# Optimization experiments

Hardware: AMD Instinct MI355X
Metric: run time of the kernel (lower is better)

## Reference

```python
import jax, jax.numpy as jnp
import numpy as np

N_NODES = 200000
N_EDGES = 3200000
NUM_GRAPHS = 100
WIN = 30
H1, H2, OUT = 500, 20, 4


def setup_inputs() -> dict:
    key = jax.random.key(0)
    ks = jax.random.split(key, 8)
    features = jax.random.normal(ks[0], (N_NODES, WIN), dtype=jnp.float32)
    src = jax.random.randint(ks[1], (N_EDGES,), 0, N_NODES, dtype=jnp.int32)
    dst = jax.random.randint(ks[2], (N_EDGES,), 0, N_NODES, dtype=jnp.int32)
    # contiguous equal-size graphs: 2000 nodes per graph -> ids sorted 0..99
    graph_ids = (jnp.arange(N_NODES, dtype=jnp.int32) // (N_NODES // NUM_GRAPHS))
    W1 = jax.random.normal(ks[3], (WIN, H1), dtype=jnp.float32) / np.sqrt(WIN)
    b1 = jnp.zeros((H1,), jnp.float32)
    W2 = jax.random.normal(ks[4], (H1, H2), dtype=jnp.float32) / np.sqrt(H1)
    b2 = jnp.zeros((H2,), jnp.float32)
    W3 = jax.random.normal(ks[5], (H2, OUT), dtype=jnp.float32) / np.sqrt(H2)
    b3 = jnp.zeros((OUT,), jnp.float32)
    return {"features": features, "src": src, "dst": dst, "graph_ids": graph_ids,
            "num_graphs": NUM_GRAPHS, "W1": W1, "b1": b1, "W2": W2, "b2": b2,
            "W3": W3, "b3": b3}


def reference(features, src, dst, graph_ids, num_graphs, W1, b1, W2, b2, W3, b3):
    N = features.shape[0]
    ones = jnp.ones(src.shape[0], dtype=features.dtype)
    # DGL GraphConv norm='both': D_out^{-1/2} on src side, D_in^{-1/2} on dst side
    deg_out = jnp.maximum(jax.ops.segment_sum(ones, src, num_segments=N), 1.0)
    deg_in = jnp.maximum(jax.ops.segment_sum(ones, dst, num_segments=N), 1.0)
    x = features * jax.lax.rsqrt(deg_out)[:, None]
    # aggregate first (in_feats < out_feats), then dense transform
    agg = jax.ops.segment_sum(x[src], dst, num_segments=N)          # [N, 30]
    agg = agg * jax.lax.rsqrt(deg_in)[:, None]
    h = jax.nn.silu(agg @ W1 + b1)                                   # [N, 500]
    pooled = jax.ops.segment_max(h, graph_ids, num_segments=num_graphs)  # [G, 500]
    y = jax.nn.silu(pooled @ W2 + b2)                                # dropout = identity (eval)
    return jax.nn.sigmoid(y @ W3 + b3)                               # [G, 4]
```

## Files before the change

kernel.cpp:

```cpp
#include <hip/hip_runtime.h>
#include <hip/hip_fp16.h>

#define WIN 30
#define H1 500
#define H1P 512
#define H2 20
#define OUTD 4
#define CS 4
#define NBIN 61440
#define NBINW (NBIN/4)
#define NCH 48
#define RPB 512
#define MAXPB 9216
#define BINCHUNK 8192
#define NBMAX 400

typedef _Float16 f16x8 __attribute__((ext_vector_type(8)));
typedef float f32x4 __attribute__((ext_vector_type(4)));

__global__ __launch_bounds__(1024) void k_hb(const int* __restrict__ src,
                                             const int* __restrict__ dst,
                                             unsigned* __restrict__ partial,
                                             int* __restrict__ gcur,
                                             unsigned* __restrict__ ebuf,
                                             int E, int NB, int NHB) {
    __shared__ unsigned h[NBINW];
    const int tid = threadIdx.x;
    if ((int)blockIdx.x < NHB) {
        const int r = blockIdx.x / NCH, c = blockIdx.x % NCH;
        const int nbase = r * NBIN;
        for (int j = tid; j < NBINW; j += 1024) h[j] = 0;
        __syncthreads();
        const int ce = ((E + NCH - 1) / NCH + 3) & ~3;
        const int start = c * ce;
        const int end = min(E, start + ce);
        for (int i = start + tid * 4; i < end; i += 1024 * 4) {
            if (i + 3 < end) {
                int4 s4 = *(const int4*)(src + i);
                unsigned d;
                d = (unsigned)(s4.x - nbase); if (d < NBIN) atomicAdd(&h[d >> 2], 1u << ((d & 3) * 8));
                d = (unsigned)(s4.y - nbase); if (d < NBIN) atomicAdd(&h[d >> 2], 1u << ((d & 3) * 8));
                d = (unsigned)(s4.z - nbase); if (d < NBIN) atomicAdd(&h[d >> 2], 1u << ((d & 3) * 8));
                d = (unsigned)(s4.w - nbase); if (d < NBIN) atomicAdd(&h[d >> 2], 1u << ((d & 3) * 8));
            } else {
                for (int k = i; k < end; ++k) {
                    unsigned d = (unsigned)(src[k] - nbase);
                    if (d < NBIN) atomicAdd(&h[d >> 2], 1u << ((d & 3) * 8));
                }
            }
        }
        __syncthreads();
        unsigned* outp = partial + (size_t)blockIdx.x * NBINW;
        for (int j = tid; j < NBINW; j += 1024) outp[j] = h[j];
    } else {
        int* cnt = (int*)h;
        int* base = (int*)h + NBMAX;
        const int bb = blockIdx.x - NHB;
        for (int j = tid; j < NB; j += 1024) cnt[j] = 0;
        __syncthreads();
        const int start = bb * BINCHUNK;
        const int end = min(E, start + BINCHUNK);
        for (int i = start + tid; i < end; i += 1024)
            atomicAdd(&cnt[dst[i] >> 9], 1);
        __syncthreads();
        for (int j = tid; j < NB; j += 1024) {
            int c = cnt[j];
            base[j] = j * MAXPB + (c ? atomicAdd(&gcur[j], c) : 0);
            cnt[j] = 0;
        }
        __syncthreads();
        for (int i = start + tid; i < end; i += 1024) {
            int d = dst[i];
            int b = d >> 9;
            int idx = atomicAdd(&cnt[b], 1);
            int pos = base[b] + idx;
            if (pos < (b + 1) * MAXPB)
                ebuf[pos] = ((unsigned)src[i] << 9) | (unsigned)(d & 511);
        }
    }
}

__global__ __launch_bounds__(256) void k_prep2(const unsigned* __restrict__ partial,
                                               const float* __restrict__ feat,
                                               const float* __restrict__ W1,
                                               __half* __restrict__ xh,
                                               __half* __restrict__ w1cm,
                                               int N, int nmb) {
    const int tid = threadIdx.x;
    if ((int)blockIdx.x == nmb) {
        for (int i = tid; i < H1P * 32; i += 256) {
            int c = i >> 5, k = i & 31;
            float v = (k < WIN && c < H1) ? W1[k * H1 + c] : 0.f;
            w1cm[i] = __float2half(v);
        }
        return;
    }
    __shared__ float rs[1024];
    {
        int w = blockIdx.x * 256 + tid;
        int node0 = 4 * w;
        int r = node0 / NBIN;
        int lw = (node0 - r * NBIN) >> 2;
        const unsigned* p = partial + (size_t)(r * NCH) * NBINW + lw;
        unsigned b0 = 0, b1 = 0, b2 = 0, b3 = 0;
        for (int c = 0; c < NCH; ++c) {
            unsigned v = p[(size_t)c * NBINW];
            b0 += v & 0xFFu; b1 += (v >> 8) & 0xFFu;
            b2 += (v >> 16) & 0xFFu; b3 += v >> 24;
        }
        rs[tid * 4 + 0] = rsqrtf((float)max((int)b0, 1));
        rs[tid * 4 + 1] = rsqrtf((float)max((int)b1, 1));
        rs[tid * 4 + 2] = rsqrtf((float)max((int)b2, 1));
        rs[tid * 4 + 3] = rsqrtf((float)max((int)b3, 1));
    }
    __syncthreads();
    const int nbase = blockIdx.x * 1024;
    for (int task = tid; task < 1024 * 4; task += 256) {
        int node_l = task >> 2;
        int node = nbase + node_l;
        if (node >= N) break;
        int c8 = (task & 3) * 8;
        float r = rs[node_l];
        float f[8];
#pragma unroll
        for (int q = 0; q < 8; ++q) {
            int d = c8 + q;
            f[q] = (d < WIN) ? feat[(size_t)node * WIN + d] * r : 0.f;
        }
        union { uint4 u4; __half2 h2[4]; } y;
        y.h2[0] = __floats2half2_rn(f[0], f[1]);
        y.h2[1] = __floats2half2_rn(f[2], f[3]);
        y.h2[2] = __floats2half2_rn(f[4], f[5]);
        y.h2[3] = __floats2half2_rn(f[6], f[7]);
        *(uint4*)(xh + (size_t)node * 32 + c8) = y.u4;
    }
}

__global__ __launch_bounds__(1024) void k_agg(const __half* __restrict__ xh,
                                              const unsigned* __restrict__ ebuf,
                                              const int* __restrict__ gcur,
                                              __half* __restrict__ agg, int N) {
    __shared__ unsigned es[MAXPB];
    __shared__ int cnt[RPB + 1];
    __shared__ int cur[RPB];
    const int tid = threadIdx.x;
    const int b = blockIdx.x;
    for (int j = tid; j < RPB; j += 1024) { cnt[j + 1] = 0; cur[j] = 0; }
    if (tid == 0) cnt[0] = 0;
    __syncthreads();
    const int ne = min(gcur[b], MAXPB);
    const unsigned* eb = ebuf + (size_t)b * MAXPB;
    for (int i = tid; i < ne; i += 1024)
        atomicAdd(&cnt[(int)(eb[i] & (RPB - 1)) + 1], 1);
    __syncthreads();
    if (tid < 64) {
        const int i0 = tid * 8;
        int s[8];
        int run = 0;
#pragma unroll
        for (int k = 0; k < 8; ++k) { run += cnt[i0 + k + 1]; s[k] = run; }
        int inc = run;
#pragma unroll
        for (int o = 1; o < 64; o <<= 1) {
            int u = __shfl_up(inc, o, 64);
            if (tid >= o) inc += u;
        }
        const int ex = inc - run;
#pragma unroll
        for (int k = 0; k < 8; ++k) cnt[i0 + k + 1] = ex + s[k];
    }
    __syncthreads();
    for (int i = tid; i < ne; i += 1024) {
        unsigned p = eb[i];
        int ld = (int)(p & (RPB - 1));
        int idx = atomicAdd(&cur[ld], 1);
        es[cnt[ld] + idx] = p;
    }
    __syncthreads();
    for (int task = tid; task < RPB * 4; task += 1024) {
        const int node_l = task >> 2;
        const int c8 = (task & 3) * 8;
        const int o0 = cnt[node_l], o1 = cnt[node_l + 1];
        float a0 = 0.f, a1 = 0.f, a2 = 0.f, a3 = 0.f;
        float a4 = 0.f, a5 = 0.f, a6 = 0.f, a7 = 0.f;
        int j = o0;
        for (; j + 3 < o1; j += 4) {
            unsigned p0 = es[j], p1 = es[j + 1], p2 = es[j + 2], p3 = es[j + 3];
            union { uint4 u4; __half2 h2[4]; } x0, x1, x2, x3;
            x0.u4 = *(const uint4*)(xh + (size_t)(p0 >> 9) * 32 + c8);
            x1.u4 = *(const uint4*)(xh + (size_t)(p1 >> 9) * 32 + c8);
            x2.u4 = *(const uint4*)(xh + (size_t)(p2 >> 9) * 32 + c8);
            x3.u4 = *(const uint4*)(xh + (size_t)(p3 >> 9) * 32 + c8);
            a0 += __low2float(x0.h2[0]) + __low2float(x1.h2[0]) + __low2float(x2.h2[0]) + __low2float(x3.h2[0]);
            a1 += __high2float(x0.h2[0]) + __high2float(x1.h2[0]) + __high2float(x2.h2[0]) + __high2float(x3.h2[0]);
            a2 += __low2float(x0.h2[1]) + __low2float(x1.h2[1]) + __low2float(x2.h2[1]) + __low2float(x3.h2[1]);
            a3 += __high2float(x0.h2[1]) + __high2float(x1.h2[1]) + __high2float(x2.h2[1]) + __high2float(x3.h2[1]);
            a4 += __low2float(x0.h2[2]) + __low2float(x1.h2[2]) + __low2float(x2.h2[2]) + __low2float(x3.h2[2]);
            a5 += __high2float(x0.h2[2]) + __high2float(x1.h2[2]) + __high2float(x2.h2[2]) + __high2float(x3.h2[2]);
            a6 += __low2float(x0.h2[3]) + __low2float(x1.h2[3]) + __low2float(x2.h2[3]) + __low2float(x3.h2[3]);
            a7 += __high2float(x0.h2[3]) + __high2float(x1.h2[3]) + __high2float(x2.h2[3]) + __high2float(x3.h2[3]);
        }
        for (; j < o1; ++j) {
            unsigned p0 = es[j];
            union { uint4 u4; __half2 h2[4]; } x0;
            x0.u4 = *(const uint4*)(xh + (size_t)(p0 >> 9) * 32 + c8);
            a0 += __low2float(x0.h2[0]);  a1 += __high2float(x0.h2[0]);
            a2 += __low2float(x0.h2[1]);  a3 += __high2float(x0.h2[1]);
            a4 += __low2float(x0.h2[2]);  a5 += __high2float(x0.h2[2]);
            a6 += __low2float(x0.h2[3]);  a7 += __high2float(x0.h2[3]);
        }
        const int node = b * RPB + node_l;
        if (node < N) {
            float deg = (float)(o1 - o0);
            float r = rsqrtf(fmaxf(deg, 1.f));
            union { uint4 u4; __half2 h2[4]; } y;
            y.h2[0] = __floats2half2_rn(a0 * r, a1 * r);
            y.h2[1] = __floats2half2_rn(a2 * r, a3 * r);
            y.h2[2] = __floats2half2_rn(a4 * r, a5 * r);
            y.h2[3] = __floats2half2_rn(a6 * r, a7 * r);
            *(uint4*)(agg + (size_t)node * 32 + c8) = y.u4;
        }
    }
}

__global__ __launch_bounds__(256) void k_gemm(const __half* __restrict__ agg,
                                              const __half* __restrict__ w1cm,
                                              const float* __restrict__ b1,
                                              float* __restrict__ pooled,
                                              int NPG, int G) {
    const int bid = blockIdx.x;
    const int g = bid / CS, c = bid % CS;
    const int tid = threadIdx.x;
    const int w = tid >> 6;
    const int l = tid & 63;
    const int lo = l & 15, hi = l >> 4;

    f16x8 bfr[8];
#pragma unroll
    for (int ct = 0; ct < 8; ++ct) {
        int col = c * 128 + ct * 16 + lo;
        bfr[ct] = *(const f16x8*)(w1cm + (size_t)col * 32 + hi * 8);
    }
    float vmax[8], vmin[8];
#pragma unroll
    for (int ct = 0; ct < 8; ++ct) { vmax[ct] = -INFINITY; vmin[ct] = INFINITY; }

    const int mts = NPG >> 4;
    for (int mt = w; mt < mts; mt += 4) {
        int node = g * NPG + mt * 16 + lo;
        f16x8 a = *(const f16x8*)(agg + (size_t)node * 32 + hi * 8);
#pragma unroll
        for (int ct = 0; ct < 8; ++ct) {
            f32x4 acc = {0.f, 0.f, 0.f, 0.f};
            acc = __builtin_amdgcn_mfma_f32_16x16x32_f16(a, bfr[ct], acc, 0, 0, 0);
#pragma unroll
            for (int q = 0; q < 4; ++q) {
                vmax[ct] = fmaxf(vmax[ct], acc[q]);
                vmin[ct] = fminf(vmin[ct], acc[q]);
            }
        }
    }
#pragma unroll
    for (int ct = 0; ct < 8; ++ct) {
        vmax[ct] = fmaxf(vmax[ct], __shfl_xor(vmax[ct], 16, 64));
        vmax[ct] = fmaxf(vmax[ct], __shfl_xor(vmax[ct], 32, 64));
        vmin[ct] = fminf(vmin[ct], __shfl_xor(vmin[ct], 16, 64));
        vmin[ct] = fminf(vmin[ct], __shfl_xor(vmin[ct], 32, 64));
    }
    __shared__ float red[2][4][8][16];
    if (hi == 0) {
#pragma unroll
        for (int ct = 0; ct < 8; ++ct) {
            red[0][w][ct][lo] = vmax[ct];
            red[1][w][ct][lo] = vmin[ct];
        }
    }
    __syncthreads();
    if (tid < 128) {
        int ct = tid >> 4, col16 = tid & 15;
        float m = fmaxf(fmaxf(red[0][0][ct][col16], red[0][1][ct][col16]),
                        fmaxf(red[0][2][ct][col16], red[0][3][ct][col16]));
        float n = fminf(fminf(red[1][0][ct][col16], red[1][1][ct][col16]),
                        fminf(red[1][2][ct][col16], red[1][3][ct][col16]));
        int col = c * 128 + ct * 16 + col16;
        float bb = (col < H1) ? b1[col] : 0.f;
        m += bb; n += bb;
        float sm = m / (1.f + __expf(-m));
        float sn = n / (1.f + __expf(-n));
        pooled[(size_t)g * H1P + col] = fmaxf(sm, sn);
    }
}

__global__ __launch_bounds__(64) void k_head(const float* __restrict__ pooled,
                                             const float* __restrict__ W2,
                                             const float* __restrict__ b2,
                                             const float* __restrict__ W3,
                                             const float* __restrict__ b3,
                                             float* __restrict__ out, int G) {
    const int g = blockIdx.x;
    const int t = threadIdx.x;
    __shared__ float y[H2];
    if (t < H2) {
        float acc = b2[t];
        for (int k = 0; k < H1; ++k)
            acc = fmaf(pooled[(size_t)g * H1P + k], W2[k * H2 + t], acc);
        y[t] = acc / (1.f + __expf(-acc));
    }
    __syncthreads();
    if (t < OUTD) {
        float acc = b3[t];
#pragma unroll
        for (int k = 0; k < H2; ++k) acc = fmaf(y[k], W3[k * OUTD + t], acc);
        out[g * OUTD + t] = 1.f / (1.f + __expf(-acc));
    }
}

static inline size_t align256(size_t x) { return (x + 255) & ~(size_t)255; }

extern "C" void kernel_launch(void* const* d_in, const int* in_sizes, int n_in,
                              void* d_out, int out_size, void* d_ws, size_t ws_size,
                              hipStream_t stream) {
    const float* feat = (const float*)d_in[0];
    const int*   src  = (const int*)d_in[1];
    const int*   dst  = (const int*)d_in[2];
    const float* W1 = (const float*)d_in[5];
    const float* b1 = (const float*)d_in[6];
    const float* W2 = (const float*)d_in[7];
    const float* b2 = (const float*)d_in[8];
    const float* W3 = (const float*)d_in[9];
    const float* b3 = (const float*)d_in[10];
    float* out = (float*)d_out;

    const int N = in_sizes[0] / WIN;
    const int E = in_sizes[1];
    const int G = out_size / OUTD;
    const int NPG = N / G;
    const int nr = (N + NBIN - 1) / NBIN;
    const int NHB = nr * NCH;
    const int NB = (N + RPB - 1) / RPB;
    const int NBB = (E + BINCHUNK - 1) / BINCHUNK;
    const int nmb = (N + 1023) / 1024;

    char* ws = (char*)d_ws;
    size_t off = 0;
    unsigned* partial = (unsigned*)(ws + off); off += align256((size_t)nr * NCH * NBINW * 4);
    __half*   xh      = (__half*)(ws + off);   off += align256((size_t)N * 32 * 2);
    __half*   w1cm    = (__half*)(ws + off);   off += align256((size_t)H1P * 32 * 2);
    __half*   agg     = (__half*)(ws + off);   off += align256((size_t)N * 32 * 2);
    float*    pooled  = (float*)(ws + off);    off += align256((size_t)G * H1P * 4);
    int*      gcur    = (int*)(ws + off);      off += align256((size_t)NB * 4);
    unsigned* ebuf    = (unsigned*)(ws + off); off += align256((size_t)NB * MAXPB * 4 + 256);
    (void)ws_size; (void)n_in;

    hipMemsetAsync(gcur, 0, (size_t)NB * 4, stream);
    k_hb<<<NHB + NBB, 1024, 0, stream>>>(src, dst, partial, gcur, ebuf, E, NB, NHB);
    k_prep2<<<nmb + 1, 256, 0, stream>>>(partial, feat, W1, xh, w1cm, N, nmb);
    k_agg<<<NB, 1024, 0, stream>>>(xh, ebuf, gcur, agg, N);
    k_gemm<<<G * CS, 256, 0, stream>>>(agg, w1cm, b1, pooled, NPG, G);
    k_head<<<G, 64, 0, stream>>>(pooled, W2, b2, W3, b3, out, G);
}
```

Baseline: 154.0 us.

## Fuse all stages into one persistent cooperative kernel with grid syncs

Merges the histogram/binning, prep, aggregation, GEMM+pool and head kernels into a single cooperative persistent kernel. Stages are separated by grid-wide barriers instead of separate launches. Every stage now uses 1024-thread blocks, and the GEMM packs four former 256-thread work units into each block. The aim is to remove per-launch overhead and inter-kernel gaps. The costs are grid-sync latency, reduced occupancy from the large shared buffer with 1024 threads, and serial looping when the grid is smaller than a stage's work count. A fallback multi-kernel path runs if the cooperative launch fails.

```diff
diff --git a/kernel.cpp b/kernel.cpp
--- a/kernel.cpp
+++ b/kernel.cpp
@@ -1,5 +1,6 @@
 #include <hip/hip_runtime.h>
 #include <hip/hip_fp16.h>
+#include <hip/hip_cooperative_groups.h>
 
 #define WIN 30
 #define H1 500
@@ -14,90 +15,94 @@
 #define MAXPB 9216
 #define BINCHUNK 8192
 #define NBMAX 400
+#define NT 1024
+
+namespace cg = cooperative_groups;
 
 typedef _Float16 f16x8 __attribute__((ext_vector_type(8)));
 typedef float f32x4 __attribute__((ext_vector_type(4)));
 
-__global__ __launch_bounds__(1024) void k_hb(const int* __restrict__ src,
-                                             const int* __restrict__ dst,
-                                             unsigned* __restrict__ partial,
-                                             int* __restrict__ gcur,
-                                             unsigned* __restrict__ ebuf,
-                                             int E, int NB, int NHB) {
-    __shared__ unsigned h[NBINW];
+
+__device__ __forceinline__ void dev_hist(int item, const int* __restrict__ src,
+                                         unsigned* __restrict__ partial, int E,
+                                         unsigned* h) {
     const int tid = threadIdx.x;
-    if ((int)blockIdx.x < NHB) {
-        const int r = blockIdx.x / NCH, c = blockIdx.x % NCH;
-        const int nbase = r * NBIN;
-        for (int j = tid; j < NBINW; j += 1024) h[j] = 0;
-        __syncthreads();
-        const int ce = ((E + NCH - 1) / NCH + 3) & ~3;
-        const int start = c * ce;
-        const int end = min(E, start + ce);
-        for (int i = start + tid * 4; i < end; i += 1024 * 4) {
-            if (i + 3 < end) {
-                int4 s4 = *(const int4*)(src + i);
-                unsigned d;
-                d = (unsigned)(s4.x - nbase); if (d < NBIN) atomicAdd(&h[d >> 2], 1u << ((d & 3) * 8));
-                d = (unsigned)(s4.y - nbase); if (d < NBIN) atomicAdd(&h[d >> 2], 1u << ((d & 3) * 8));
-                d = (unsigned)(s4.z - nbase); if (d < NBIN) atomicAdd(&h[d >> 2], 1u << ((d & 3) * 8));
-                d = (unsigned)(s4.w - nbase); if (d < NBIN) atomicAdd(&h[d >> 2], 1u << ((d & 3) * 8));
-            } else {
-                for (int k = i; k < end; ++k) {
-                    unsigned d = (unsigned)(src[k] - nbase);
-                    if (d < NBIN) atomicAdd(&h[d >> 2], 1u << ((d & 3) * 8));
-                }
+    const int r = item / NCH, c = item % NCH;
+    const int nbase = r * NBIN;
+    for (int j = tid; j < NBINW; j += NT) h[j] = 0;
+    __syncthreads();
+    const int ce = ((E + NCH - 1) / NCH + 3) & ~3;
+    const int start = c * ce;
+    const int end = min(E, start + ce);
+    for (int i = start + tid * 4; i < end; i += NT * 4) {
+        if (i + 3 < end) {
+            int4 s4 = *(const int4*)(src + i);
+            unsigned d;
+            d = (unsigned)(s4.x - nbase); if (d < NBIN) atomicAdd(&h[d >> 2], 1u << ((d & 3) * 8));
+            d = (unsigned)(s4.y - nbase); if (d < NBIN) atomicAdd(&h[d >> 2], 1u << ((d & 3) * 8));
+            d = (unsigned)(s4.z - nbase); if (d < NBIN) atomicAdd(&h[d >> 2], 1u << ((d & 3) * 8));
+            d = (unsigned)(s4.w - nbase); if (d < NBIN) atomicAdd(&h[d >> 2], 1u << ((d & 3) * 8));
+        } else {
+            for (int k = i; k < end; ++k) {
+                unsigned d = (unsigned)(src[k] - nbase);
+                if (d < NBIN) atomicAdd(&h[d >> 2], 1u << ((d & 3) * 8));
             }
         }
-        __syncthreads();
-        unsigned* outp = partial + (size_t)blockIdx.x * NBINW;
-        for (int j = tid; j < NBINW; j += 1024) outp[j] = h[j];
-    } else {
-        int* cnt = (int*)h;
-        int* base = (int*)h + NBMAX;
-        const int bb = blockIdx.x - NHB;
-        for (int j = tid; j < NB; j += 1024) cnt[j] = 0;
-        __syncthreads();
-        const int start = bb * BINCHUNK;
-        const int end = min(E, start + BINCHUNK);
-        for (int i = start + tid; i < end; i += 1024)
-            atomicAdd(&cnt[dst[i] >> 9], 1);
-        __syncthreads();
-        for (int j = tid; j < NB; j += 1024) {
-            int c = cnt[j];
-            base[j] = j * MAXPB + (c ? atomicAdd(&gcur[j], c) : 0);
-            cnt[j] = 0;
-        }
-        __syncthreads();
-        for (int i = start + tid; i < end; i += 1024) {
-            int d = dst[i];
-            int b = d >> 9;
-            int idx = atomicAdd(&cnt[b], 1);
-            int pos = base[b] + idx;
-            if (pos < (b + 1) * MAXPB)
-                ebuf[pos] = ((unsigned)src[i] << 9) | (unsigned)(d & 511);
-        }
-    }
-}
-
-__global__ __launch_bounds__(256) void k_prep2(const unsigned* __restrict__ partial,
-                                               const float* __restrict__ feat,
-                                               const float* __restrict__ W1,
-                                               __half* __restrict__ xh,
-                                               __half* __restrict__ w1cm,
-                                               int N, int nmb) {
+    }
+    __syncthreads();
+    unsigned* outp = partial + (size_t)item * NBINW;
+    for (int j = tid; j < NBINW; j += NT) outp[j] = h[j];
+}
+
+__device__ __forceinline__ void dev_bin(int bb, const int* __restrict__ src,
+                                        const int* __restrict__ dst,
+                                        int* __restrict__ gcur,
+                                        unsigned* __restrict__ ebuf,
+                                        int E, int NB, unsigned* lds) {
+    int* cnt = (int*)lds;
+    int* base = (int*)lds + NBMAX;
     const int tid = threadIdx.x;
-    if ((int)blockIdx.x == nmb) {
-        for (int i = tid; i < H1P * 32; i += 256) {
+    for (int j = tid; j < NB; j += NT) cnt[j] = 0;
+    __syncthreads();
+    const int start = bb * BINCHUNK;
+    const int end = min(E, start + BINCHUNK);
+    for (int i = start + tid; i < end; i += NT)
+        atomicAdd(&cnt[dst[i] >> 9], 1);
+    __syncthreads();
+    for (int j = tid; j < NB; j += NT) {
+        int c = cnt[j];
+        base[j] = j * MAXPB + (c ? atomicAdd(&gcur[j], c) : 0);
+        cnt[j] = 0;
+    }
+    __syncthreads();
+    for (int i = start + tid; i < end; i += NT) {
+        int d = dst[i];
+        int b = d >> 9;
+        int idx = atomicAdd(&cnt[b], 1);
+        int pos = base[b] + idx;
+        if (pos < (b + 1) * MAXPB)
+            ebuf[pos] = ((unsigned)src[i] << 9) | (unsigned)(d & 511);
+    }
+}
+
+__device__ __forceinline__ void dev_prep(int item, const unsigned* __restrict__ partial,
+                                         const float* __restrict__ feat,
+                                         const float* __restrict__ W1,
+                                         __half* __restrict__ xh,
+                                         __half* __restrict__ w1cm,
+                                         int N, int nmb, unsigned* lds) {
+    const int tid = threadIdx.x;
+    if (item == nmb) {
+        for (int i = tid; i < H1P * 32; i += NT) {
             int c = i >> 5, k = i & 31;
             float v = (k < WIN && c < H1) ? W1[k * H1 + c] : 0.f;
             w1cm[i] = __float2half(v);
         }
         return;
     }
-    __shared__ float rs[1024];
-    {
-        int w = blockIdx.x * 256 + tid;
+    float* rs = (float*)lds;
+    if (tid < 256) {
+        int w = item * 256 + tid;
         int node0 = 4 * w;
         int r = node0 / NBIN;
         int lw = (node0 - r * NBIN) >> 2;
@@ -114,8 +119,8 @@
         rs[tid * 4 + 3] = rsqrtf((float)max((int)b3, 1));
     }
     __syncthreads();
-    const int nbase = blockIdx.x * 1024;
-    for (int task = tid; task < 1024 * 4; task += 256) {
+    const int nbase = item * 1024;
+    for (int task = tid; task < 1024 * 4; task += NT) {
         int node_l = task >> 2;
         int node = nbase + node_l;
         if (node >= N) break;
@@ -136,21 +141,21 @@
     }
 }
 
-__global__ __launch_bounds__(1024) void k_agg(const __half* __restrict__ xh,
-                                              const unsigned* __restrict__ ebuf,
-                                              const int* __restrict__ gcur,
-                                              __half* __restrict__ agg, int N) {
-    __shared__ unsigned es[MAXPB];
-    __shared__ int cnt[RPB + 1];
-    __shared__ int cur[RPB];
+__device__ __forceinline__ void dev_agg(int b, const __half* __restrict__ xh,
+                                        const unsigned* __restrict__ ebuf,
+                                        const int* __restrict__ gcur,
+                                        __half* __restrict__ agg, int N,
+                                        unsigned* lds) {
+    unsigned* es = lds;
+    int* cnt = (int*)(lds + MAXPB);
+    int* cur = (int*)(lds + MAXPB) + RPB + 1;
     const int tid = threadIdx.x;
-    const int b = blockIdx.x;
-    for (int j = tid; j < RPB; j += 1024) { cnt[j + 1] = 0; cur[j] = 0; }
+    for (int j = tid; j < RPB; j += NT) { cnt[j + 1] = 0; cur[j] = 0; }
     if (tid == 0) cnt[0] = 0;
     __syncthreads();
     const int ne = min(gcur[b], MAXPB);
     const unsigned* eb = ebuf + (size_t)b * MAXPB;
-    for (int i = tid; i < ne; i += 1024)
+    for (int i = tid; i < ne; i += NT)
         atomicAdd(&cnt[(int)(eb[i] & (RPB - 1)) + 1], 1);
     __syncthreads();
     if (tid < 64) {
@@ -170,14 +175,14 @@
         for (int k = 0; k < 8; ++k) cnt[i0 + k + 1] = ex + s[k];
     }
     __syncthreads();
-    for (int i = tid; i < ne; i += 1024) {
+    for (int i = tid; i < ne; i += NT) {
         unsigned p = eb[i];
         int ld = (int)(p & (RPB - 1));
         int idx = atomicAdd(&cur[ld], 1);
         es[cnt[ld] + idx] = p;
     }
     __syncthreads();
-    for (int task = tid; task < RPB * 4; task += 1024) {
+    for (int task = tid; task < RPB * 4; task += NT) {
         const int node_l = task >> 2;
         const int c8 = (task & 3) * 8;
         const int o0 = cnt[node_l], o1 = cnt[node_l + 1];
@@ -223,17 +228,20 @@
     }
 }
 
-__global__ __launch_bounds__(256) void k_gemm(const __half* __restrict__ agg,
-                                              const __half* __restrict__ w1cm,
-                                              const float* __restrict__ b1,
-                                              float* __restrict__ pooled,
-                                              int NPG, int G) {
-    const int bid = blockIdx.x;
-    const int g = bid / CS, c = bid % CS;
+__device__ __forceinline__ void dev_gemm(int vb4, const __half* __restrict__ agg,
+                                         const __half* __restrict__ w1cm,
+                                         const float* __restrict__ b1,
+                                         float* __restrict__ pooled,
+                                         int NPG, float* red) {
     const int tid = threadIdx.x;
-    const int w = tid >> 6;
-    const int l = tid & 63;
+    const int q = tid >> 8;
+    const int lt = tid & 255;
+    const int vb = vb4 * 4 + q;
+    const int g = vb / CS, c = vb % CS;
+    const int w = lt >> 6;
+    const int l = lt & 63;
     const int lo = l & 15, hi = l >> 4;
+    float* rq = red + q * 1024;
 
     f16x8 bfr[8];
 #pragma unroll
@@ -254,9 +262,9 @@
             f32x4 acc = {0.f, 0.f, 0.f, 0.f};
             acc = __builtin_amdgcn_mfma_f32_16x16x32_f16(a, bfr[ct], acc, 0, 0, 0);
 #pragma unroll
-            for (int q = 0; q < 4; ++q) {
-                vmax[ct] = fmaxf(vmax[ct], acc[q]);
-                vmin[ct] = fminf(vmin[ct], acc[q]);
+            for (int p = 0; p < 4; ++p) {
+                vmax[ct] = fmaxf(vmax[ct], acc[p]);
+                vmin[ct] = fminf(vmin[ct], acc[p]);
             }
         }
     }
@@ -267,21 +275,24 @@
         vmin[ct] = fminf(vmin[ct], __shfl_xor(vmin[ct], 16, 64));
         vmin[ct] = fminf(vmin[ct], __shfl_xor(vmin[ct], 32, 64));
     }
-    __shared__ float red[2][4][8][16];
     if (hi == 0) {
 #pragma unroll
         for (int ct = 0; ct < 8; ++ct) {
-            red[0][w][ct][lo] = vmax[ct];
-            red[1][w][ct][lo] = vmin[ct];
-        }
-    }
-    __syncthreads();
-    if (tid < 128) {
-        int ct = tid >> 4, col16 = tid & 15;
-        float m = fmaxf(fmaxf(red[0][0][ct][col16], red[0][1][ct][col16]),
-                        fmaxf(red[0][2][ct][col16], red[0][3][ct][col16]));
-        float n = fminf(fminf(red[1][0][ct][col16], red[1][1][ct][col16]),
-                        fminf(red[1][2][ct][col16], red[1][3][ct][col16]));
+            rq[((0 * 4 + w) * 8 + ct) * 16 + lo] = vmax[ct];
+            rq[((1 * 4 + w) * 8 + ct) * 16 + lo] = vmin[ct];
+        }
+    }
+    __syncthreads();
+    if (lt < 128) {
+        int ct = lt >> 4, col16 = lt & 15;
+        float m = fmaxf(fmaxf(rq[((0 * 4 + 0) * 8 + ct) * 16 + col16],
+                              rq[((0 * 4 + 1) * 8 + ct) * 16 + col16]),
+                        fmaxf(rq[((0 * 4 + 2) * 8 + ct) * 16 + col16],
+                              rq[((0 * 4 + 3) * 8 + ct) * 16 + col16]));
+        float n = fminf(fminf(rq[((1 * 4 + 0) * 8 + ct) * 16 + col16],
+                              rq[((1 * 4 + 1) * 8 + ct) * 16 + col16]),
+                        fminf(rq[((1 * 4 + 2) * 8 + ct) * 16 + col16],
+                              rq[((1 * 4 + 3) * 8 + ct) * 16 + col16]));
         int col = c * 128 + ct * 16 + col16;
         float bb = (col < H1) ? b1[col] : 0.f;
         m += bb; n += bb;
@@ -291,15 +302,13 @@
     }
 }
 
-__global__ __launch_bounds__(64) void k_head(const float* __restrict__ pooled,
-                                             const float* __restrict__ W2,
-                                             const float* __restrict__ b2,
-                                             const float* __restrict__ W3,
-                                             const float* __restrict__ b3,
-                                             float* __restrict__ out, int G) {
-    const int g = blockIdx.x;
+__device__ __forceinline__ void dev_head(int g, const float* __restrict__ pooled,
+                                         const float* __restrict__ W2,
+                                         const float* __restrict__ b2,
+                                         const float* __restrict__ W3,
+                                         const float* __restrict__ b3,
+                                         float* __restrict__ out, float* y) {
     const int t = threadIdx.x;
-    __shared__ float y[H2];
     if (t < H2) {
         float acc = b2[t];
         for (int k = 0; k < H1; ++k)
@@ -315,14 +324,78 @@
     }
 }
 
+__global__ __launch_bounds__(NT, 8) void k_mega(const int* src, const int* dst,
+        const float* feat, const float* W1, const float* b1, const float* W2,
+        const float* b2, const float* W3, const float* b3, float* out,
+        unsigned* partial, __half* xh, __half* w1cm, __half* agg, float* pooled,
+        int* gcur, unsigned* ebuf,
+        int E, int N, int NB, int NHB, int NBB, int nmb, int NPG, int G) {
+    cg::grid_group gg = cg::this_grid();
+    __shared__ unsigned lds[NBINW];
+    const int nb = gridDim.x;
+    for (int it = blockIdx.x; it < NHB + NBB; it += nb) {
+        if (it < NHB) dev_hist(it, src, partial, E, lds);
+        else dev_bin(it - NHB, src, dst, gcur, ebuf, E, NB, lds);
+        __syncthreads();
+    }
+    gg.sync();
+    for (int it = blockIdx.x; it < nmb + 1; it += nb) {
+        dev_prep(it, partial, feat, W1, xh, w1cm, N, nmb, lds);
+        __syncthreads();
+    }
+    gg.sync();
+    for (int b = blockIdx.x; b < NB; b += nb) {
+        dev_agg(b, xh, ebuf, gcur, agg, N, lds);
+        __syncthreads();
+    }
+    gg.sync();
+    const int nv4 = (G * CS) / 4;
+    for (int v4 = blockIdx.x; v4 < nv4; v4 += nb) {
+        dev_gemm(v4, agg, w1cm, b1, pooled, NPG, (float*)lds);
+        __syncthreads();
+    }
+    gg.sync();
+    for (int g = blockIdx.x; g < G; g += nb) {
+        dev_head(g, pooled, W2, b2, W3, b3, out, (float*)lds);
+        __syncthreads();
+    }
+}
+
+__global__ __launch_bounds__(NT) void k_hb(const int* src, const int* dst,
+        unsigned* partial, int* gcur, unsigned* ebuf, int E, int NB, int NHB) {
+    __shared__ unsigned lds[NBINW];
+    if ((int)blockIdx.x < NHB) dev_hist(blockIdx.x, src, partial, E, lds);
+    else dev_bin(blockIdx.x - NHB, src, dst, gcur, ebuf, E, NB, lds);
+}
+__global__ __launch_bounds__(NT) void k_prep2(const unsigned* partial, const float* feat,
+        const float* W1, __half* xh, __half* w1cm, int N, int nmb) {
+    __shared__ unsigned lds[1024];
+    dev_prep(blockIdx.x, partial, feat, W1, xh, w1cm, N, nmb, lds);
+}
+__global__ __launch_bounds__(NT) void k_agg(const __half* xh, const unsigned* ebuf,
+        const int* gcur, __half* agg, int N) {
+    __shared__ unsigned lds[MAXPB + 1152];
+    dev_agg(blockIdx.x, xh, ebuf, gcur, agg, N, lds);
+}
+__global__ __launch_bounds__(NT) void k_gemm4(const __half* agg, const __half* w1cm,
+        const float* b1, float* pooled, int NPG) {
+    __shared__ float red[4096];
+    dev_gemm(blockIdx.x, agg, w1cm, b1, pooled, NPG, red);
+}
+__global__ __launch_bounds__(NT) void k_head(const float* pooled, const float* W2,
+        const float* b2, const float* W3, const float* b3, float* out) {
+    __shared__ float y[H2];
+    dev_head(blockIdx.x, pooled, W2, b2, W3, b3, out, y);
+}
+
 static inline size_t align256(size_t x) { return (x + 255) & ~(size_t)255; }
 
 extern "C" void kernel_launch(void* const* d_in, const int* in_sizes, int n_in,
                               void* d_out, int out_size, void* d_ws, size_t ws_size,
                               hipStream_t stream) {
-    const float* feat = (const float*)d_in[0];
     const int*   src  = (const int*)d_in[1];
     const int*   dst  = (const int*)d_in[2];
+    const float* feat = (const float*)d_in[0];
     const float* W1 = (const float*)d_in[5];
     const float* b1 = (const float*)d_in[6];
     const float* W2 = (const float*)d_in[7];
@@ -331,15 +404,16 @@
     const float* b3 = (const float*)d_in[10];
     float* out = (float*)d_out;
 
-    const int N = in_sizes[0] / WIN;
     const int E = in_sizes[1];
-    const int G = out_size / OUTD;
-    const int NPG = N / G;
+    int N = in_sizes[0] / WIN;
+    int G = out_size / OUTD;
+    int NPG = N / G;
     const int nr = (N + NBIN - 1) / NBIN;
-    const int NHB = nr * NCH;
-    const int NB = (N + RPB - 1) / RPB;
-    const int NBB = (E + BINCHUNK - 1) / BINCHUNK;
-    const int nmb = (N + 1023) / 1024;
+    int NHB = nr * NCH;
+    int NB = (N + RPB - 1) / RPB;
+    int NBB = (E + BINCHUNK - 1) / BINCHUNK;
+    int nmb = (N + 1023) / 1024;
+    int Ev = E;
 
     char* ws = (char*)d_ws;
     size_t off = 0;
@@ -353,9 +427,27 @@
     (void)ws_size; (void)n_in;
 
     hipMemsetAsync(gcur, 0, (size_t)NB * 4, stream);
-    k_hb<<<NHB + NBB, 1024, 0, stream>>>(src, dst, partial, gcur, ebuf, E, NB, NHB);
-    k_prep2<<<nmb + 1, 256, 0, stream>>>(partial, feat, W1, xh, w1cm, N, nmb);
-    k_agg<<<NB, 1024, 0, stream>>>(xh, ebuf, gcur, agg, N);
-    k_gemm<<<G * CS, 256, 0, stream>>>(agg, w1cm, b1, pooled, NPG, G);
-    k_head<<<G, 64, 0, stream>>>(pooled, W2, b2, W3, b3, out, G);
-}
+
+    int occ = 0;
+    hipError_t qe = hipOccupancyMaxActiveBlocksPerMultiprocessor(&occ, k_mega, NT, 0);
+    if (qe != hipSuccess || occ < 1) occ = 1;
+    int grid = occ * 256;
+    if (grid > 512) grid = 512;
+
+    void* args[] = {
+        (void*)&src, (void*)&dst, (void*)&feat, (void*)&W1, (void*)&b1,
+        (void*)&W2, (void*)&b2, (void*)&W3, (void*)&b3, (void*)&out,
+        (void*)&partial, (void*)&xh, (void*)&w1cm, (void*)&agg, (void*)&pooled,
+        (void*)&gcur, (void*)&ebuf,
+        (void*)&Ev, (void*)&N, (void*)&NB, (void*)&NHB, (void*)&NBB,
+        (void*)&nmb, (void*)&NPG, (void*)&G };
+    hipError_t le = hipLaunchCooperativeKernel(k_mega, dim3(grid), dim3(NT),
+                                               args, 0, stream);
+    if (le != hipSuccess) {
+        k_hb<<<NHB + NBB, NT, 0, stream>>>(src, dst, partial, gcur, ebuf, E, NB, NHB);
+        k_prep2<<<nmb + 1, NT, 0, stream>>>(partial, feat, W1, xh, w1cm, N, nmb);
+        k_agg<<<NB, NT, 0, stream>>>(xh, ebuf, gcur, agg, N);
+        k_gemm4<<<(G * CS) / 4, NT, 0, stream>>>(agg, w1cm, b1, pooled, NPG);
+        k_head<<<G, NT, 0, stream>>>(pooled, W2, b2, W3, b3, out);
+    }
+}
```

New measurement: 302.7 us. 96.5% more time.

## Sort aggregation edges by source range so block phases gather from localized source nodes

Applied to the files above, without the earlier changes.

The shared-memory counting sort in the aggregation kernel now keys edges by (source range from the top bits, local destination) instead of destination alone, giving 2048 buckets and a two-level block-wide scan. Each thread then accumulates two destination nodes across four source-range phases, with block-wide barriers between phases so all waves gather from the same quarter of the source feature array together. The aim is better L2/cache locality for the random source-row gathers. It costs a larger scan, extra barriers and more live accumulator registers per thread, and it depends on the source id being packed in the upper bits of the edge word.

```diff
diff --git a/kernel.cpp b/kernel.cpp
--- a/kernel.cpp
+++ b/kernel.cpp
@@ -14,6 +14,8 @@
 #define MAXPB 9216
 #define BINCHUNK 8192
 #define NBMAX 400
+#define NRANGE 4
+#define NKEY (NRANGE * RPB)
 
 typedef _Float16 f16x8 __attribute__((ext_vector_type(8)));
 typedef float f32x4 __attribute__((ext_vector_type(4)));
@@ -136,88 +138,132 @@
     }
 }
 
+#define ACC8(o0, o1, c8, a0,a1,a2,a3,a4,a5,a6,a7)                              \
+    {                                                                          \
+        int j = (o0);                                                          \
+        for (; j + 3 < (o1); j += 4) {                                         \
+            unsigned p0 = es[j], p1 = es[j+1], p2 = es[j+2], p3 = es[j+3];     \
+            union { uint4 u4; __half2 h2[4]; } x0, x1, x2, x3;                 \
+            x0.u4 = *(const uint4*)(xh + (size_t)(p0 >> 9) * 32 + (c8));       \
+            x1.u4 = *(const uint4*)(xh + (size_t)(p1 >> 9) * 32 + (c8));       \
+            x2.u4 = *(const uint4*)(xh + (size_t)(p2 >> 9) * 32 + (c8));       \
+            x3.u4 = *(const uint4*)(xh + (size_t)(p3 >> 9) * 32 + (c8));       \
+            a0 += __low2float(x0.h2[0]) + __low2float(x1.h2[0]) + __low2float(x2.h2[0]) + __low2float(x3.h2[0]); \
+            a1 += __high2float(x0.h2[0]) + __high2float(x1.h2[0]) + __high2float(x2.h2[0]) + __high2float(x3.h2[0]); \
+            a2 += __low2float(x0.h2[1]) + __low2float(x1.h2[1]) + __low2float(x2.h2[1]) + __low2float(x3.h2[1]); \
+            a3 += __high2float(x0.h2[1]) + __high2float(x1.h2[1]) + __high2float(x2.h2[1]) + __high2float(x3.h2[1]); \
+            a4 += __low2float(x0.h2[2]) + __low2float(x1.h2[2]) + __low2float(x2.h2[2]) + __low2float(x3.h2[2]); \
+            a5 += __high2float(x0.h2[2]) + __high2float(x1.h2[2]) + __high2float(x2.h2[2]) + __high2float(x3.h2[2]); \
+            a6 += __low2float(x0.h2[3]) + __low2float(x1.h2[3]) + __low2float(x2.h2[3]) + __low2float(x3.h2[3]); \
+            a7 += __high2float(x0.h2[3]) + __high2float(x1.h2[3]) + __high2float(x2.h2[3]) + __high2float(x3.h2[3]); \
+        }                                                                      \
+        for (; j < (o1); ++j) {                                                \
+            unsigned p0 = es[j];                                               \
+            union { uint4 u4; __half2 h2[4]; } x0;                             \
+            x0.u4 = *(const uint4*)(xh + (size_t)(p0 >> 9) * 32 + (c8));       \
+            a0 += __low2float(x0.h2[0]);  a1 += __high2float(x0.h2[0]);        \
+            a2 += __low2float(x0.h2[1]);  a3 += __high2float(x0.h2[1]);        \
+            a4 += __low2float(x0.h2[2]);  a5 += __high2float(x0.h2[2]);        \
+            a6 += __low2float(x0.h2[3]);  a7 += __high2float(x0.h2[3]);        \
+        }                                                                      \
+    }
+
 __global__ __launch_bounds__(1024) void k_agg(const __half* __restrict__ xh,
                                               const unsigned* __restrict__ ebuf,
                                               const int* __restrict__ gcur,
                                               __half* __restrict__ agg, int N) {
     __shared__ unsigned es[MAXPB];
-    __shared__ int cnt[RPB + 1];
-    __shared__ int cur[RPB];
+    __shared__ int cnt[NKEY + 1];
+    __shared__ int cur[NKEY];
+    __shared__ int wsum[16];
     const int tid = threadIdx.x;
     const int b = blockIdx.x;
-    for (int j = tid; j < RPB; j += 1024) { cnt[j + 1] = 0; cur[j] = 0; }
+    for (int j = tid; j < NKEY; j += 1024) { cnt[j + 1] = 0; cur[j] = 0; }
     if (tid == 0) cnt[0] = 0;
     __syncthreads();
     const int ne = min(gcur[b], MAXPB);
     const unsigned* eb = ebuf + (size_t)b * MAXPB;
-    for (int i = tid; i < ne; i += 1024)
-        atomicAdd(&cnt[(int)(eb[i] & (RPB - 1)) + 1], 1);
-    __syncthreads();
-    if (tid < 64) {
-        const int i0 = tid * 8;
-        int s[8];
-        int run = 0;
-#pragma unroll
-        for (int k = 0; k < 8; ++k) { run += cnt[i0 + k + 1]; s[k] = run; }
-        int inc = run;
+    for (int i = tid; i < ne; i += 1024) {
+        unsigned p = eb[i];
+        int key = (int)(p >> 25) * RPB + (int)(p & (RPB - 1));
+        atomicAdd(&cnt[key + 1], 1);
+    }
+    __syncthreads();
+    {
+        int v0 = cnt[2 * tid + 1], v1 = cnt[2 * tid + 2];
+        int t = v0 + v1;
+        int inc = t;
 #pragma unroll
         for (int o = 1; o < 64; o <<= 1) {
             int u = __shfl_up(inc, o, 64);
-            if (tid >= o) inc += u;
-        }
-        const int ex = inc - run;
-#pragma unroll
-        for (int k = 0; k < 8; ++k) cnt[i0 + k + 1] = ex + s[k];
+            if ((tid & 63) >= o) inc += u;
+        }
+        if ((tid & 63) == 63) wsum[tid >> 6] = inc;
+        __syncthreads();
+        if (tid < 16) {
+            int w = wsum[tid];
+            int wi = w;
+#pragma unroll
+            for (int o = 1; o < 16; o <<= 1) {
+                int u = __shfl_up(wi, o, 64);
+                if (tid >= o) wi += u;
+            }
+            wsum[tid] = wi - w;
+        }
+        __syncthreads();
+        int ex = wsum[tid >> 6] + (inc - t);
+        cnt[2 * tid + 1] = ex + v0;
+        cnt[2 * tid + 2] = ex + v0 + v1;
     }
     __syncthreads();
     for (int i = tid; i < ne; i += 1024) {
         unsigned p = eb[i];
-        int ld = (int)(p & (RPB - 1));
-        int idx = atomicAdd(&cur[ld], 1);
-        es[cnt[ld] + idx] = p;
-    }
-    __syncthreads();
-    for (int task = tid; task < RPB * 4; task += 1024) {
-        const int node_l = task >> 2;
-        const int c8 = (task & 3) * 8;
-        const int o0 = cnt[node_l], o1 = cnt[node_l + 1];
-        float a0 = 0.f, a1 = 0.f, a2 = 0.f, a3 = 0.f;
-        float a4 = 0.f, a5 = 0.f, a6 = 0.f, a7 = 0.f;
-        int j = o0;
-        for (; j + 3 < o1; j += 4) {
-            unsigned p0 = es[j], p1 = es[j + 1], p2 = es[j + 2], p3 = es[j + 3];
-            union { uint4 u4; __half2 h2[4]; } x0, x1, x2, x3;
-            x0.u4 = *(const uint4*)(xh + (size_t)(p0 >> 9) * 32 + c8);
-            x1.u4 = *(const uint4*)(xh + (size_t)(p1 >> 9) * 32 + c8);
-            x2.u4 = *(const uint4*)(xh + (size_t)(p2 >> 9) * 32 + c8);
-            x3.u4 = *(const uint4*)(xh + (size_t)(p3 >> 9) * 32 + c8);
-            a0 += __low2float(x0.h2[0]) + __low2float(x1.h2[0]) + __low2float(x2.h2[0]) + __low2float(x3.h2[0]);
-            a1 += __high2float(x0.h2[0]) + __high2float(x1.h2[0]) + __high2float(x2.h2[0]) + __high2float(x3.h2[0]);
-            a2 += __low2float(x0.h2[1]) + __low2float(x1.h2[1]) + __low2float(x2.h2[1]) + __low2float(x3.h2[1]);
-            a3 += __high2float(x0.h2[1]) + __high2float(x1.h2[1]) + __high2float(x2.h2[1]) + __high2float(x3.h2[1]);
-            a4 += __low2float(x0.h2[2]) + __low2float(x1.h2[2]) + __low2float(x2.h2[2]) + __low2float(x3.h2[2]);
-            a5 += __high2float(x0.h2[2]) + __high2float(x1.h2[2]) + __high2float(x2.h2[2]) + __high2float(x3.h2[2]);
-            a6 += __low2float(x0.h2[3]) + __low2float(x1.h2[3]) + __low2float(x2.h2[3]) + __low2float(x3.h2[3]);
-            a7 += __high2float(x0.h2[3]) + __high2float(x1.h2[3]) + __high2float(x2.h2[3]) + __high2float(x3.h2[3]);
-        }
-        for (; j < o1; ++j) {
-            unsigned p0 = es[j];
-            union { uint4 u4; __half2 h2[4]; } x0;
-            x0.u4 = *(const uint4*)(xh + (size_t)(p0 >> 9) * 32 + c8);
-            a0 += __low2float(x0.h2[0]);  a1 += __high2float(x0.h2[0]);
-            a2 += __low2float(x0.h2[1]);  a3 += __high2float(x0.h2[1]);
-            a4 += __low2float(x0.h2[2]);  a5 += __high2float(x0.h2[2]);
-            a6 += __low2float(x0.h2[3]);  a7 += __high2float(x0.h2[3]);
-        }
-        const int node = b * RPB + node_l;
+        int key = (int)(p >> 25) * RPB + (int)(p & (RPB - 1));
+        int idx = atomicAdd(&cur[key], 1);
+        es[cnt[key] + idx] = p;
+    }
+    __syncthreads();
+    const int n0 = tid >> 2;
+    const int n1 = n0 + 256;
+    const int c8 = (tid & 3) * 8;
+    float A0=0.f,A1=0.f,A2=0.f,A3=0.f,A4=0.f,A5=0.f,A6=0.f,A7=0.f;
+    float B0=0.f,B1=0.f,B2=0.f,B3=0.f,B4=0.f,B5=0.f,B6=0.f,B7=0.f;
+    int degA = 0, degB = 0;
+#pragma unroll
+    for (int r = 0; r < NRANGE; ++r) {
+        {
+            int o0 = cnt[r * RPB + n0], o1 = cnt[r * RPB + n0 + 1];
+            degA += o1 - o0;
+            ACC8(o0, o1, c8, A0,A1,A2,A3,A4,A5,A6,A7);
+        }
+        {
+            int o0 = cnt[r * RPB + n1], o1 = cnt[r * RPB + n1 + 1];
+            degB += o1 - o0;
+            ACC8(o0, o1, c8, B0,B1,B2,B3,B4,B5,B6,B7);
+        }
+        __syncthreads();
+    }
+    {
+        int node = b * RPB + n0;
         if (node < N) {
-            float deg = (float)(o1 - o0);
-            float r = rsqrtf(fmaxf(deg, 1.f));
+            float rr = rsqrtf(fmaxf((float)degA, 1.f));
             union { uint4 u4; __half2 h2[4]; } y;
-            y.h2[0] = __floats2half2_rn(a0 * r, a1 * r);
-            y.h2[1] = __floats2half2_rn(a2 * r, a3 * r);
-            y.h2[2] = __floats2half2_rn(a4 * r, a5 * r);
-            y.h2[3] = __floats2half2_rn(a6 * r, a7 * r);
+            y.h2[0] = __floats2half2_rn(A0 * rr, A1 * rr);
+            y.h2[1] = __floats2half2_rn(A2 * rr, A3 * rr);
+            y.h2[2] = __floats2half2_rn(A4 * rr, A5 * rr);
+            y.h2[3] = __floats2half2_rn(A6 * rr, A7 * rr);
+            *(uint4*)(agg + (size_t)node * 32 + c8) = y.u4;
+        }
+    }
+    {
+        int node = b * RPB + n1;
+        if (node < N) {
+            float rr = rsqrtf(fmaxf((float)degB, 1.f));
+            union { uint4 u4; __half2 h2[4]; } y;
+            y.h2[0] = __floats2half2_rn(B0 * rr, B1 * rr);
+            y.h2[1] = __floats2half2_rn(B2 * rr, B3 * rr);
+            y.h2[2] = __floats2half2_rn(B4 * rr, B5 * rr);
+            y.h2[3] = __floats2half2_rn(B6 * rr, B7 * rr);
             *(uint4*)(agg + (size_t)node * 32 + c8) = y.u4;
         }
     }
```

Result: faster. 149.9 us (-2.7%).
